# Performance work log

Measured on AMD Instinct MI355X. Metric: run time of the kernel, lower is better.

Reference implementation:

```python
import jax, jax.numpy as jnp
import numpy as np

WEIGHT_GRADIENT = 0.05
EPS = 1e-6


def _normalize(q, eps):
    # torch F.normalize: q / max(||q||, eps)
    n = jnp.sqrt(jnp.sum(q * q, axis=1, keepdims=True))
    return q / jnp.maximum(n, eps)


def _grad_mag(q, eps):
    # depthwise conv with [-1,1] kernels == finite differences, then replicate-pad
    gx = q[..., :, 1:] - q[..., :, :-1]          # (B,4,H,W-1)
    gy = q[..., 1:, :] - q[..., :-1, :]          # (B,4,H-1,W)
    gx = jnp.pad(gx, ((0, 0), (0, 0), (0, 0), (0, 1)), mode='edge')
    gy = jnp.pad(gy, ((0, 0), (0, 0), (0, 1), (0, 0)), mode='edge')
    return jnp.sqrt(gx * gx + gy * gy + eps)


def setup_inputs() -> dict:
    key = jax.random.key(0)
    k1, k2, k3 = jax.random.split(key, 3)
    B, H, W, S = 16, 256, 256, 24
    q_pred = jax.random.normal(k1, (B, 4, H, W), dtype=jnp.float32)
    q_target = jax.random.normal(k2, (B, 4, H, W), dtype=jnp.float32)
    syms = jax.random.normal(k3, (S, 4), dtype=jnp.float32)
    syms = syms / jnp.linalg.norm(syms, axis=1, keepdims=True)  # unit quaternions
    return {"q_pred": q_pred, "q_target": q_target, "syms": syms}


def reference(q_pred, q_target, syms, eps=EPS):
    # (B,4,H,W) -> (N,4)
    qp = _normalize(q_pred.transpose(0, 2, 3, 1).reshape(-1, 4), eps)
    qt = _normalize(q_target.transpose(0, 2, 3, 1).reshape(-1, 4), eps)
    w1, x1, y1, z1 = qp[:, 0], qp[:, 1], qp[:, 2], qp[:, 3]
    w2, x2, y2, z2 = qt[:, 0], qt[:, 1], qt[:, 2], qt[:, 3]
    # relative quaternion r = qt * conj(qp)
    rw = w2 * w1 + x2 * x1 + y2 * y1 + z2 * z1
    rx = -w2 * x1 + x2 * w1 - y2 * z1 + z2 * y1
    ry = -w2 * y1 + x2 * z1 + y2 * w1 - z2 * x1
    rz = -w2 * z1 - x2 * y1 + y2 * x1 + z2 * w1
    r4 = jnp.stack([rw, rx, ry, rz], axis=1)                 # (N,4)
    signs = jnp.array([1.0, -1.0, -1.0, -1.0], dtype=syms.dtype)
    # w_dist[n,s] = rw*s_w - rx*s_x - ry*s_y - rz*s_z
    w_dist = jnp.einsum('nc,sc->ns', r4, syms * signs)       # (N,S)
    max_w = jnp.max(jnp.abs(w_dist), axis=1)
    max_w = jnp.clip(max_w, -(1.0 - eps), 1.0 - eps)
    loss_rot = jnp.mean(2.0 * jnp.arccos(max_w))
    gp = _grad_mag(q_pred, eps)
    gt = _grad_mag(q_target, eps)
    loss_grad = jnp.mean(jnp.abs(gp - gt))
    return loss_rot + WEIGHT_GRADIENT * loss_grad
```

## Files before the change

kernel.cpp:

```cpp
#include <hip/hip_runtime.h>
#include <math.h>

constexpr int Hc = 256;
constexpr int Wc = 256;
constexpr float EPSf = 1e-6f;

__device__ __forceinline__ float comp(const float4& v, int p) {
    return p == 0 ? v.x : p == 1 ? v.y : p == 2 ? v.z : v.w;
}

__global__ __launch_bounds__(256) void sym_loss_main(
    const float* __restrict__ qp,
    const float* __restrict__ qt,
    const float* __restrict__ syms,
    int S,
    float2* __restrict__ partial)
{
    __shared__ float4 s_sym[32];
    if (threadIdx.x < S) {
        float4 v;
        v.x =  syms[4 * threadIdx.x + 0];
        v.y = -syms[4 * threadIdx.x + 1];
        v.z = -syms[4 * threadIdx.x + 2];
        v.w = -syms[4 * threadIdx.x + 3];
        s_sym[threadIdx.x] = v;
    }
    __syncthreads();

    int t    = blockIdx.x * 256 + threadIdx.x;
    int lane = t & 63;
    int row  = t >> 6;
    int b    = row >> 8;
    int h    = row & (Hc - 1);
    int w0   = lane << 2;

    int idx0 = (b << 18) + (h << 8) + w0;
    int dy = (h == Hc - 1) ? -Wc : Wc;

    float4 pc[4], tc[4];
    float gsum = 0.0f;

    #pragma unroll
    for (int c = 0; c < 4; ++c) {
        int idx = idx0 + (c << 16);
        float4 C  = *(const float4*)(qp + idx);
        float4 Y  = *(const float4*)(qp + idx + dy);
        float4 Ct = *(const float4*)(qt + idx);
        float4 Yt = *(const float4*)(qt + idx + dy);
        pc[c] = C; tc[c] = Ct;

        float nx  = __shfl_down(C.x, 1, 64);
        float nxt = __shfl_down(Ct.x, 1, 64);
        float px3 = (lane == 63) ? C.z  : nx;
        float tx3 = (lane == 63) ? Ct.z : nxt;

        float gx, gy, gp, gt_;
        gx = C.y - C.x;  gy = Y.x - C.x;
        gp  = sqrtf(fmaf(gx, gx, fmaf(gy, gy, EPSf)));
        gx = Ct.y - Ct.x; gy = Yt.x - Ct.x;
        gt_ = sqrtf(fmaf(gx, gx, fmaf(gy, gy, EPSf)));
        gsum += fabsf(gp - gt_);

        gx = C.z - C.y;  gy = Y.y - C.y;
        gp  = sqrtf(fmaf(gx, gx, fmaf(gy, gy, EPSf)));
        gx = Ct.z - Ct.y; gy = Yt.y - Ct.y;
        gt_ = sqrtf(fmaf(gx, gx, fmaf(gy, gy, EPSf)));
        gsum += fabsf(gp - gt_);

        gx = C.w - C.z;  gy = Y.z - C.z;
        gp  = sqrtf(fmaf(gx, gx, fmaf(gy, gy, EPSf)));
        gx = Ct.w - Ct.z; gy = Yt.z - Ct.z;
        gt_ = sqrtf(fmaf(gx, gx, fmaf(gy, gy, EPSf)));
        gsum += fabsf(gp - gt_);

        gx = px3 - C.w;  gy = Y.w - C.w;
        gp  = sqrtf(fmaf(gx, gx, fmaf(gy, gy, EPSf)));
        gx = tx3 - Ct.w; gy = Yt.w - Ct.w;
        gt_ = sqrtf(fmaf(gx, gx, fmaf(gy, gy, EPSf)));
        gsum += fabsf(gp - gt_);
    }

    float rw[4], rx[4], ry[4], rz[4];
    #pragma unroll
    for (int p = 0; p < 4; ++p) {
        float a0 = comp(pc[0], p), a1 = comp(pc[1], p),
              a2 = comp(pc[2], p), a3 = comp(pc[3], p);
        float b0 = comp(tc[0], p), b1 = comp(tc[1], p),
              b2 = comp(tc[2], p), b3 = comp(tc[3], p);

        float n1 = sqrtf(fmaf(a0, a0, fmaf(a1, a1, fmaf(a2, a2, a3 * a3))));
        float n2 = sqrtf(fmaf(b0, b0, fmaf(b1, b1, fmaf(b2, b2, b3 * b3))));
        float i1 = 1.0f / fmaxf(n1, EPSf);
        float i2 = 1.0f / fmaxf(n2, EPSf);
        float w1 = a0 * i1, x1 = a1 * i1, y1 = a2 * i1, z1 = a3 * i1;
        float w2 = b0 * i2, x2 = b1 * i2, y2 = b2 * i2, z2 = b3 * i2;

        rw[p] =  w2 * w1 + x2 * x1 + y2 * y1 + z2 * z1;
        rx[p] = -w2 * x1 + x2 * w1 - y2 * z1 + z2 * y1;
        ry[p] = -w2 * y1 + x2 * z1 + y2 * w1 - z2 * x1;
        rz[p] = -w2 * z1 - x2 * y1 + y2 * x1 + z2 * w1;
    }

    float maxw[4] = {0.f, 0.f, 0.f, 0.f};
    for (int s = 0; s < S; ++s) {
        float4 sv = s_sym[s];
        #pragma unroll
        for (int p = 0; p < 4; ++p) {
            float d = fmaf(rz[p], sv.w,
                      fmaf(ry[p], sv.z,
                      fmaf(rx[p], sv.y, rw[p] * sv.x)));
            maxw[p] = fmaxf(maxw[p], fabsf(d));
        }
    }
    float rot = 0.0f;
    #pragma unroll
    for (int p = 0; p < 4; ++p)
        rot += 2.0f * acosf(fminf(maxw[p], 1.0f - EPSf));

    #pragma unroll
    for (int off = 32; off > 0; off >>= 1) {
        rot  += __shfl_down(rot,  off, 64);
        gsum += __shfl_down(gsum, off, 64);
    }
    __shared__ float s_r[4], s_g[4];
    int wid = threadIdx.x >> 6;
    if ((threadIdx.x & 63) == 0) { s_r[wid] = rot; s_g[wid] = gsum; }
    __syncthreads();
    if (threadIdx.x == 0) {
        float2 out;
        out.x = s_r[0] + s_r[1] + s_r[2] + s_r[3];
        out.y = s_g[0] + s_g[1] + s_g[2] + s_g[3];
        partial[blockIdx.x] = out;
    }
}

__global__ __launch_bounds__(256) void sym_loss_reduce(
    const float2* __restrict__ partial, int nblocks,
    float* __restrict__ out, double invNP, double invNE)
{
    double r = 0.0, g = 0.0;
    for (int i = threadIdx.x; i < nblocks; i += 256) {
        float2 p = partial[i];
        r += (double)p.x;
        g += (double)p.y;
    }
    #pragma unroll
    for (int off = 32; off > 0; off >>= 1) {
        r += __shfl_down(r, off, 64);
        g += __shfl_down(g, off, 64);
    }
    __shared__ double s_r[4], s_g[4];
    int wid = threadIdx.x >> 6;
    if ((threadIdx.x & 63) == 0) { s_r[wid] = r; s_g[wid] = g; }
    __syncthreads();
    if (threadIdx.x == 0) {
        double rr = s_r[0] + s_r[1] + s_r[2] + s_r[3];
        double gg = s_g[0] + s_g[1] + s_g[2] + s_g[3];
        out[0] = (float)(rr * invNP + 0.05 * gg * invNE);
    }
}

extern "C" void kernel_launch(void* const* d_in, const int* in_sizes, int n_in,
                              void* d_out, int out_size, void* d_ws, size_t ws_size,
                              hipStream_t stream)
{
    const float* qp   = (const float*)d_in[0];
    const float* qt   = (const float*)d_in[1];
    const float* syms = (const float*)d_in[2];

    int S  = in_sizes[2] / 4;
    int NP = in_sizes[0] / 4;
    int nthreads = NP / 4;
    int nblocks  = nthreads / 256;

    float2* partial = (float2*)d_ws;

    sym_loss_main<<<nblocks, 256, 0, stream>>>(qp, qt, syms, S, partial);

    double invNP = 1.0 / (double)NP;
    double invNE = 1.0 / ((double)NP * 4.0);
    sym_loss_reduce<<<1, 256, 0, stream>>>(partial, nblocks, (float*)d_out,
                                           invNP, invNE);
}
```

Before: 86.34 us.

## Specialize symmetry loop for S=24, hoist all loads, replace shuffle with direct neighbor load

Templates the main kernel on S and fully unrolls the symmetry loop, reading symmetry quaternions directly from global (uniform, likely scalar loads) instead of staging them in LDS with a barrier. All global loads are issued up front, and the cross-lane shuffle for the right neighbor is replaced by an extra scalar load. rsq replaces sqrt+divide in normalization, which drops the eps clamp, and launch bounds request 4 blocks per CU. A generic fallback kernel handles other S; the trade is higher register pressure and slightly different numerics near zero norms.

Result: no change. 84.72 us (-1.9%).

```diff
diff --git a/kernel.cpp b/kernel.cpp
--- a/kernel.cpp
+++ b/kernel.cpp
@@ -9,24 +9,13 @@
     return p == 0 ? v.x : p == 1 ? v.y : p == 2 ? v.z : v.w;
 }
 
-__global__ __launch_bounds__(256) void sym_loss_main(
+template<int S>
+__global__ __launch_bounds__(256, 4) void sym_loss_main(
     const float* __restrict__ qp,
     const float* __restrict__ qt,
     const float* __restrict__ syms,
-    int S,
     float2* __restrict__ partial)
 {
-    __shared__ float4 s_sym[32];
-    if (threadIdx.x < S) {
-        float4 v;
-        v.x =  syms[4 * threadIdx.x + 0];
-        v.y = -syms[4 * threadIdx.x + 1];
-        v.z = -syms[4 * threadIdx.x + 2];
-        v.w = -syms[4 * threadIdx.x + 3];
-        s_sym[threadIdx.x] = v;
-    }
-    __syncthreads();
-
     int t    = blockIdx.x * 256 + threadIdx.x;
     int lane = t & 63;
     int row  = t >> 6;
@@ -36,79 +25,83 @@
 
     int idx0 = (b << 18) + (h << 8) + w0;
     int dy = (h == Hc - 1) ? -Wc : Wc;
-
-    float4 pc[4], tc[4];
+    int xo = (lane == 63) ? 2 : 4;
+
+    float4 Cp[4], Yp[4], Ct[4], Yt[4];
+    float  xp[4], xt[4];
+    #pragma unroll
+    for (int c = 0; c < 4; ++c) {
+        int idx = idx0 + (c << 16);
+        Cp[c] = *(const float4*)(qp + idx);
+        Yp[c] = *(const float4*)(qp + idx + dy);
+        xp[c] = qp[idx + xo];
+        Ct[c] = *(const float4*)(qt + idx);
+        Yt[c] = *(const float4*)(qt + idx + dy);
+        xt[c] = qt[idx + xo];
+    }
+
     float gsum = 0.0f;
-
-    #pragma unroll
-    for (int c = 0; c < 4; ++c) {
-        int idx = idx0 + (c << 16);
-        float4 C  = *(const float4*)(qp + idx);
-        float4 Y  = *(const float4*)(qp + idx + dy);
-        float4 Ct = *(const float4*)(qt + idx);
-        float4 Yt = *(const float4*)(qt + idx + dy);
-        pc[c] = C; tc[c] = Ct;
-
-        float nx  = __shfl_down(C.x, 1, 64);
-        float nxt = __shfl_down(Ct.x, 1, 64);
-        float px3 = (lane == 63) ? C.z  : nx;
-        float tx3 = (lane == 63) ? Ct.z : nxt;
-
-        float gx, gy, gp, gt_;
-        gx = C.y - C.x;  gy = Y.x - C.x;
-        gp  = sqrtf(fmaf(gx, gx, fmaf(gy, gy, EPSf)));
-        gx = Ct.y - Ct.x; gy = Yt.x - Ct.x;
-        gt_ = sqrtf(fmaf(gx, gx, fmaf(gy, gy, EPSf)));
-        gsum += fabsf(gp - gt_);
-
-        gx = C.z - C.y;  gy = Y.y - C.y;
-        gp  = sqrtf(fmaf(gx, gx, fmaf(gy, gy, EPSf)));
-        gx = Ct.z - Ct.y; gy = Yt.y - Ct.y;
-        gt_ = sqrtf(fmaf(gx, gx, fmaf(gy, gy, EPSf)));
-        gsum += fabsf(gp - gt_);
-
-        gx = C.w - C.z;  gy = Y.z - C.z;
-        gp  = sqrtf(fmaf(gx, gx, fmaf(gy, gy, EPSf)));
-        gx = Ct.w - Ct.z; gy = Yt.z - Ct.z;
-        gt_ = sqrtf(fmaf(gx, gx, fmaf(gy, gy, EPSf)));
-        gsum += fabsf(gp - gt_);
-
-        gx = px3 - C.w;  gy = Y.w - C.w;
-        gp  = sqrtf(fmaf(gx, gx, fmaf(gy, gy, EPSf)));
-        gx = tx3 - Ct.w; gy = Yt.w - Ct.w;
-        gt_ = sqrtf(fmaf(gx, gx, fmaf(gy, gy, EPSf)));
-        gsum += fabsf(gp - gt_);
-    }
-
-    float rw[4], rx[4], ry[4], rz[4];
+    #pragma unroll
+    for (int c = 0; c < 4; ++c) {
+        float4 C = Cp[c], Y = Yp[c], D = Ct[c], Z = Yt[c];
+        float gx, gy, a, e;
+        gx = C.y - C.x; gy = Y.x - C.x;
+        a = sqrtf(fmaf(gx, gx, fmaf(gy, gy, EPSf)));
+        gx = D.y - D.x; gy = Z.x - D.x;
+        e = sqrtf(fmaf(gx, gx, fmaf(gy, gy, EPSf)));
+        gsum += fabsf(a - e);
+
+        gx = C.z - C.y; gy = Y.y - C.y;
+        a = sqrtf(fmaf(gx, gx, fmaf(gy, gy, EPSf)));
+        gx = D.z - D.y; gy = Z.y - D.y;
+        e = sqrtf(fmaf(gx, gx, fmaf(gy, gy, EPSf)));
+        gsum += fabsf(a - e);
+
+        gx = C.w - C.z; gy = Y.z - C.z;
+        a = sqrtf(fmaf(gx, gx, fmaf(gy, gy, EPSf)));
+        gx = D.w - D.z; gy = Z.z - D.z;
+        e = sqrtf(fmaf(gx, gx, fmaf(gy, gy, EPSf)));
+        gsum += fabsf(a - e);
+
+        gx = xp[c] - C.w; gy = Y.w - C.w;
+        a = sqrtf(fmaf(gx, gx, fmaf(gy, gy, EPSf)));
+        gx = xt[c] - D.w; gy = Z.w - D.w;
+        e = sqrtf(fmaf(gx, gx, fmaf(gy, gy, EPSf)));
+        gsum += fabsf(a - e);
+    }
+
+    float rw[4], nx[4], ny[4], nz[4];
     #pragma unroll
     for (int p = 0; p < 4; ++p) {
-        float a0 = comp(pc[0], p), a1 = comp(pc[1], p),
-              a2 = comp(pc[2], p), a3 = comp(pc[3], p);
-        float b0 = comp(tc[0], p), b1 = comp(tc[1], p),
-              b2 = comp(tc[2], p), b3 = comp(tc[3], p);
-
-        float n1 = sqrtf(fmaf(a0, a0, fmaf(a1, a1, fmaf(a2, a2, a3 * a3))));
-        float n2 = sqrtf(fmaf(b0, b0, fmaf(b1, b1, fmaf(b2, b2, b3 * b3))));
-        float i1 = 1.0f / fmaxf(n1, EPSf);
-        float i2 = 1.0f / fmaxf(n2, EPSf);
+        float a0 = comp(Cp[0], p), a1 = comp(Cp[1], p),
+              a2 = comp(Cp[2], p), a3 = comp(Cp[3], p);
+        float b0 = comp(Ct[0], p), b1 = comp(Ct[1], p),
+              b2 = comp(Ct[2], p), b3 = comp(Ct[3], p);
+
+        float ss1 = fmaf(a0, a0, fmaf(a1, a1, fmaf(a2, a2, a3 * a3)));
+        float ss2 = fmaf(b0, b0, fmaf(b1, b1, fmaf(b2, b2, b3 * b3)));
+        float i1 = __builtin_amdgcn_rsqf(ss1);
+        float i2 = __builtin_amdgcn_rsqf(ss2);
         float w1 = a0 * i1, x1 = a1 * i1, y1 = a2 * i1, z1 = a3 * i1;
         float w2 = b0 * i2, x2 = b1 * i2, y2 = b2 * i2, z2 = b3 * i2;
 
         rw[p] =  w2 * w1 + x2 * x1 + y2 * y1 + z2 * z1;
-        rx[p] = -w2 * x1 + x2 * w1 - y2 * z1 + z2 * y1;
-        ry[p] = -w2 * y1 + x2 * z1 + y2 * w1 - z2 * x1;
-        rz[p] = -w2 * z1 - x2 * y1 + y2 * x1 + z2 * w1;
-    }
-
+        float rx = -w2 * x1 + x2 * w1 - y2 * z1 + z2 * y1;
+        float ry = -w2 * y1 + x2 * z1 + y2 * w1 - z2 * x1;
+        float rz = -w2 * z1 - x2 * y1 + y2 * x1 + z2 * w1;
+        nx[p] = -rx; ny[p] = -ry; nz[p] = -rz;
+    }
+
+    const float4* __restrict__ sv4 = (const float4*)syms;
     float maxw[4] = {0.f, 0.f, 0.f, 0.f};
+    #pragma unroll
     for (int s = 0; s < S; ++s) {
-        float4 sv = s_sym[s];
+        float4 sv = sv4[s];
         #pragma unroll
         for (int p = 0; p < 4; ++p) {
-            float d = fmaf(rz[p], sv.w,
-                      fmaf(ry[p], sv.z,
-                      fmaf(rx[p], sv.y, rw[p] * sv.x)));
+            float d = fmaf(nz[p], sv.w,
+                      fmaf(ny[p], sv.z,
+                      fmaf(nx[p], sv.y, rw[p] * sv.x)));
             maxw[p] = fmaxf(maxw[p], fabsf(d));
         }
     }
@@ -127,10 +120,117 @@
     if ((threadIdx.x & 63) == 0) { s_r[wid] = rot; s_g[wid] = gsum; }
     __syncthreads();
     if (threadIdx.x == 0) {
-        float2 out;
-        out.x = s_r[0] + s_r[1] + s_r[2] + s_r[3];
-        out.y = s_g[0] + s_g[1] + s_g[2] + s_g[3];
-        partial[blockIdx.x] = out;
+        float2 o;
+        o.x = s_r[0] + s_r[1] + s_r[2] + s_r[3];
+        o.y = s_g[0] + s_g[1] + s_g[2] + s_g[3];
+        partial[blockIdx.x] = o;
+    }
+}
+
+__global__ __launch_bounds__(256) void sym_loss_generic(
+    const float* __restrict__ qp,
+    const float* __restrict__ qt,
+    const float* __restrict__ syms,
+    int S,
+    float2* __restrict__ partial)
+{
+    int t    = blockIdx.x * 256 + threadIdx.x;
+    int lane = t & 63;
+    int row  = t >> 6;
+    int b    = row >> 8;
+    int h    = row & (Hc - 1);
+    int w0   = lane << 2;
+    int idx0 = (b << 18) + (h << 8) + w0;
+    int dy = (h == Hc - 1) ? -Wc : Wc;
+    int xo = (lane == 63) ? 2 : 4;
+
+    float4 Cp[4], Yp[4], Ct[4], Yt[4];
+    float  xp[4], xt[4];
+    #pragma unroll
+    for (int c = 0; c < 4; ++c) {
+        int idx = idx0 + (c << 16);
+        Cp[c] = *(const float4*)(qp + idx);
+        Yp[c] = *(const float4*)(qp + idx + dy);
+        xp[c] = qp[idx + xo];
+        Ct[c] = *(const float4*)(qt + idx);
+        Yt[c] = *(const float4*)(qt + idx + dy);
+        xt[c] = qt[idx + xo];
+    }
+    float gsum = 0.0f;
+    #pragma unroll
+    for (int c = 0; c < 4; ++c) {
+        float4 C = Cp[c], Y = Yp[c], D = Ct[c], Z = Yt[c];
+        float gx, gy, a, e;
+        gx = C.y - C.x; gy = Y.x - C.x;
+        a = sqrtf(fmaf(gx, gx, fmaf(gy, gy, EPSf)));
+        gx = D.y - D.x; gy = Z.x - D.x;
+        e = sqrtf(fmaf(gx, gx, fmaf(gy, gy, EPSf)));
+        gsum += fabsf(a - e);
+        gx = C.z - C.y; gy = Y.y - C.y;
+        a = sqrtf(fmaf(gx, gx, fmaf(gy, gy, EPSf)));
+        gx = D.z - D.y; gy = Z.y - D.y;
+        e = sqrtf(fmaf(gx, gx, fmaf(gy, gy, EPSf)));
+        gsum += fabsf(a - e);
+        gx = C.w - C.z; gy = Y.z - C.z;
+        a = sqrtf(fmaf(gx, gx, fmaf(gy, gy, EPSf)));
+        gx = D.w - D.z; gy = Z.z - D.z;
+        e = sqrtf(fmaf(gx, gx, fmaf(gy, gy, EPSf)));
+        gsum += fabsf(a - e);
+        gx = xp[c] - C.w; gy = Y.w - C.w;
+        a = sqrtf(fmaf(gx, gx, fmaf(gy, gy, EPSf)));
+        gx = xt[c] - D.w; gy = Z.w - D.w;
+        e = sqrtf(fmaf(gx, gx, fmaf(gy, gy, EPSf)));
+        gsum += fabsf(a - e);
+    }
+    float rw[4], nx[4], ny[4], nz[4];
+    #pragma unroll
+    for (int p = 0; p < 4; ++p) {
+        float a0 = comp(Cp[0], p), a1 = comp(Cp[1], p),
+              a2 = comp(Cp[2], p), a3 = comp(Cp[3], p);
+        float b0 = comp(Ct[0], p), b1 = comp(Ct[1], p),
+              b2 = comp(Ct[2], p), b3 = comp(Ct[3], p);
+        float ss1 = fmaf(a0, a0, fmaf(a1, a1, fmaf(a2, a2, a3 * a3)));
+        float ss2 = fmaf(b0, b0, fmaf(b1, b1, fmaf(b2, b2, b3 * b3)));
+        float i1 = __builtin_amdgcn_rsqf(ss1);
+        float i2 = __builtin_amdgcn_rsqf(ss2);
+        float w1 = a0 * i1, x1 = a1 * i1, y1 = a2 * i1, z1 = a3 * i1;
+        float w2 = b0 * i2, x2 = b1 * i2, y2 = b2 * i2, z2 = b3 * i2;
+        rw[p] =  w2 * w1 + x2 * x1 + y2 * y1 + z2 * z1;
+        float rx = -w2 * x1 + x2 * w1 - y2 * z1 + z2 * y1;
+        float ry = -w2 * y1 + x2 * z1 + y2 * w1 - z2 * x1;
+        float rz = -w2 * z1 - x2 * y1 + y2 * x1 + z2 * w1;
+        nx[p] = -rx; ny[p] = -ry; nz[p] = -rz;
+    }
+    const float4* __restrict__ sv4 = (const float4*)syms;
+    float maxw[4] = {0.f, 0.f, 0.f, 0.f};
+    for (int s = 0; s < S; ++s) {
+        float4 sv = sv4[s];
+        #pragma unroll
+        for (int p = 0; p < 4; ++p) {
+            float d = fmaf(nz[p], sv.w,
+                      fmaf(ny[p], sv.z,
+                      fmaf(nx[p], sv.y, rw[p] * sv.x)));
+            maxw[p] = fmaxf(maxw[p], fabsf(d));
+        }
+    }
+    float rot = 0.0f;
+    #pragma unroll
+    for (int p = 0; p < 4; ++p)
+        rot += 2.0f * acosf(fminf(maxw[p], 1.0f - EPSf));
+    #pragma unroll
+    for (int off = 32; off > 0; off >>= 1) {
+        rot  += __shfl_down(rot,  off, 64);
+        gsum += __shfl_down(gsum, off, 64);
+    }
+    __shared__ float s_r[4], s_g[4];
+    int wid = threadIdx.x >> 6;
+    if ((threadIdx.x & 63) == 0) { s_r[wid] = rot; s_g[wid] = gsum; }
+    __syncthreads();
+    if (threadIdx.x == 0) {
+        float2 o;
+        o.x = s_r[0] + s_r[1] + s_r[2] + s_r[3];
+        o.y = s_g[0] + s_g[1] + s_g[2] + s_g[3];
+        partial[blockIdx.x] = o;
     }
 }
 
@@ -175,7 +275,11 @@
 
     float2* partial = (float2*)d_ws;
 
-    sym_loss_main<<<nblocks, 256, 0, stream>>>(qp, qt, syms, S, partial);
+    if (S == 24) {
+        sym_loss_main<24><<<nblocks, 256, 0, stream>>>(qp, qt, syms, partial);
+    } else {
+        sym_loss_generic<<<nblocks, 256, 0, stream>>>(qp, qt, syms, S, partial);
+    }
 
     double invNP = 1.0 / (double)NP;
     double invNE = 1.0 / ((double)NP * 4.0);
```
